# Optimization experiments

Measured on AMD Instinct MI355X. Metric: run time of the kernel, lower is better.

Reference implementation:

```python
import jax, jax.numpy as jnp
import numpy as np

S, M, E, K, C = 4096, 512, 16, 2, 128
H1, H2, H3 = 500, 500, 2000
SAMPLE = int(np.percentile(np.arange(S), 90))  # = 3685, matches int(np.percentile(idx_set, 90))
KMUL, KNUM = 2.0, 5


def setup_inputs() -> dict:
    key = jax.random.key(0)
    ks = jax.random.split(key, 8)
    def init(k, shape, fan):
        return (jax.random.normal(k, shape, jnp.float32) / np.float32(np.sqrt(fan)))
    inp = {
        'x': jax.random.normal(ks[0], (S, M), jnp.float32),
        'noise': jax.random.uniform(ks[1], (S, E), jnp.float32),
        'Wr': jnp.zeros((E, M), jnp.float32),  # router weight is zeroed in reset_parameters
        'W1': init(ks[2], (E, H1, M), M), 'b1': jnp.zeros((E, H1), jnp.float32),
        'W2': init(ks[3], (E, H2, H1), H1), 'b2': jnp.zeros((E, H2), jnp.float32),
        'W3': init(ks[4], (E, H3, H2), H2), 'b3': jnp.zeros((E, H3), jnp.float32),
        'W4': init(ks[5], (E, C, H3), H3), 'b4': jnp.zeros((E, C), jnp.float32),
    }
    rng = np.random.RandomState(0)
    npairs = K * (K - 1) // 2
    inp['idx1'] = jnp.asarray(np.stack([rng.choice(S, SAMPLE, replace=False) for _ in range(npairs)]).astype(np.int32))
    inp['idx2'] = jnp.asarray(np.stack([rng.choice(S, SAMPLE, replace=False) for _ in range(npairs)]).astype(np.int32))
    return inp


def _mmd(source, target):
    # Gaussian-kernel MMD, same math as MMD_loss (fix_sigma=None path).
    ns = source.shape[0]
    n = ns + target.shape[0]
    total = jnp.concatenate([source, target], axis=0)            # [n, d]
    sq = jnp.sum(total * total, axis=-1)
    d2 = sq[:, None] + sq[None, :] - 2.0 * (total @ total.T)     # [n, n] squared L2
    bw = jax.lax.stop_gradient(d2).sum() / (n * n - n)           # .data in torch => stop_gradient
    bw = bw / (KMUL ** (KNUM // 2))
    kern = jnp.zeros_like(d2)
    for i in range(KNUM):
        kern = kern + jnp.exp(-d2 / (bw * (KMUL ** i)))
    xx = kern[:ns, :ns]
    yy = kern[ns:, ns:]
    xy = kern[:ns, ns:]
    yx = kern[ns:, :ns]
    return jnp.mean(xx + yy - xy - yx)


def _forward(x, noise, Wr, W1, b1, W2, b2, W3, b3, W4, b4, idx1, idx2):
    select = x @ Wr.T + noise                                    # [S, E]
    gate, index = jax.lax.top_k(select, K)                       # [S, K]
    mask = jax.nn.one_hot(index, E, dtype=select.dtype)          # [S, K, E]
    density = mask.mean(axis=-2)                                 # [S, E]
    density_proxy = select.mean(axis=-2)                         # [E]
    balance_loss = jnp.mean(density_proxy * density) * float(E ** 2)
    mask_flat = mask.sum(axis=-1)                                # [S, K] (all ones)
    combine = jnp.transpose(gate[..., None] * mask_flat[..., None] * mask, (0, 2, 1))  # [S, E, K]
    dispatch = (combine != 0).astype(combine.dtype)              # bool().to(dtype)
    select0 = dispatch
    expert_inputs = jnp.einsum('sm,sec->ecm', x, dispatch)       # [E, K, M]
    h = jax.nn.relu(jnp.einsum('ecm,ehm->ech', expert_inputs, W1) + b1[:, None, :])
    h = jax.nn.relu(jnp.einsum('ech,egh->ecg', h, W2) + b2[:, None, :])
    h = jax.nn.relu(jnp.einsum('ecg,efg->ecf', h, W3) + b3[:, None, :])
    eout = jnp.einsum('ecf,edf->ecd', h, W4) + b4[:, None, :]    # [E, K, C]
    middle = jnp.transpose(jnp.einsum('sec,ecm->scm', combine, eout), (1, 0, 2))  # [K, S, C]
    output = jnp.einsum('sec,ecm->sm', combine, eout)            # [S, C]
    dist_loss = jnp.float32(0.0)
    p = 0
    for i in range(K):
        for j in range(i + 1, K):
            dist_loss = dist_loss - _mmd(middle[i][idx1[p]], middle[j][idx2[p]])
            p += 1
    return output, select0, balance_loss, dist_loss


def reference(x, noise, Wr, W1, b1, W2, b2, W3, b3, W4, b4, idx1, idx2):
    return _forward(x, noise, Wr, W1, b1, W2, b2, W3, b3, W4, b4, idx1, idx2)
```

## Files before the change

### kernel.cpp

```cpp
#include <hip/hip_runtime.h>

constexpr int S = 4096, M = 512, E = 16, CC = 128;
constexpr int H1 = 500, H2 = 500, H3 = 2000;
constexpr int TB = 256;

__global__ void k_route(const float* __restrict__ x, const float* __restrict__ noise,
                        const float* __restrict__ Wr, int* __restrict__ i0, int* __restrict__ i1,
                        float* __restrict__ g0, float* __restrict__ g1,
                        float* __restrict__ sel0, float* __restrict__ selpart,
                        int* __restrict__ counters) {
  if (blockIdx.x == 0 && threadIdx.x == 0) { counters[0] = 0; }
  int wid = threadIdx.x >> 6, lane = threadIdx.x & 63;
  int s = blockIdx.x * 4 + wid;
  const float* xr = x + (size_t)s * M;
  float xv[8];
#pragma unroll
  for (int c = 0; c < 8; ++c) xv[c] = xr[lane + 64 * c];
  float v[E];
#pragma unroll
  for (int e = 0; e < E; ++e) {
    const float* wr = Wr + (size_t)e * M;
    float acc = 0.f;
#pragma unroll
    for (int c = 0; c < 8; ++c) acc = fmaf(xv[c], wr[lane + 64 * c], acc);
#pragma unroll
    for (int off = 32; off; off >>= 1) acc += __shfl_xor(acc, off);
    v[e] = acc + noise[s * E + e];
  }
  int a0 = 0; float m0 = v[0];
#pragma unroll
  for (int e = 1; e < E; ++e) if (v[e] > m0) { m0 = v[e]; a0 = e; }
  int a1 = -1; float m1 = -3.4e38f;
#pragma unroll
  for (int e = 0; e < E; ++e) if (e != a0 && v[e] > m1) { m1 = v[e]; a1 = e; }
  __shared__ float vsh[4][16];
  if (lane < 16) vsh[wid][lane] = v[lane];
  if (lane == 0) { i0[s] = a0; i1[s] = a1; g0[s] = m0; g1[s] = m1; }
  if (lane < 16) {
    int e = lane;
    sel0[(size_t)s * 32 + e * 2 + 0] = (e == a0 && m0 != 0.f) ? 1.f : 0.f;
    sel0[(size_t)s * 32 + e * 2 + 1] = (e == a1 && m1 != 0.f) ? 1.f : 0.f;
  }
  __syncthreads();
  if (threadIdx.x < 16) {
    int e = threadIdx.x;
    selpart[blockIdx.x * 16 + e] = vsh[0][e] + vsh[1][e] + vsh[2][e] + vsh[3][e];
  }
}

__global__ void k_balance(const float* __restrict__ selpart, const int* __restrict__ i0,
                          const int* __restrict__ i1, float* __restrict__ outb) {
  __shared__ double part[512];
  __shared__ float dpl[E];
  int t = threadIdx.x;
  int e = t & 15, r0 = t >> 4;
  double acc = 0.0;
  for (int b = r0; b < 1024; b += 32) acc += (double)selpart[b * 16 + e];
  part[t] = acc;
  __syncthreads();
  for (int off = 256; off >= 16; off >>= 1) {
    if (t < off) part[t] += part[t + off];
    __syncthreads();
  }
  if (t < E) dpl[t] = (float)(part[t] / (double)S);
  __syncthreads();
  double acc2 = 0.0;
  for (int s = t; s < S; s += 512) acc2 += 0.5 * ((double)dpl[i0[s]] + (double)dpl[i1[s]]);
  part[t] = acc2;
  __syncthreads();
  for (int off = 256; off; off >>= 1) {
    if (t < off) part[t] += part[t + off];
    __syncthreads();
  }
  if (t == 0) outb[0] = (float)(part[0] / 256.0);
}

__global__ void k_lists(const int* __restrict__ i0, const int* __restrict__ i1,
                        const float* __restrict__ g0, const float* __restrict__ g1,
                        int* __restrict__ list, int* __restrict__ cnt) {
  int ek = blockIdx.x;
  int k = ek & 1, e = ek >> 1;
  const int* route = k ? i1 : i0;
  const float* gg = k ? g1 : g0;
  __shared__ int base_s;
  __shared__ int wsum[4];
  int t = threadIdx.x;
  int lane = t & 63, w = t >> 6;
  if (t == 0) base_s = 0;
  __syncthreads();
  for (int s0 = 0; s0 < S; s0 += 256) {
    int s = s0 + t;
    bool flag = (route[s] == e) && (gg[s] != 0.f);
    unsigned long long m = __ballot(flag);
    int within = __popcll(m & ((1ull << lane) - 1ull));
    if (lane == 0) wsum[w] = __popcll(m);
    __syncthreads();
    int wbase = base_s;
    for (int i = 0; i < w; ++i) wbase += wsum[i];
    if (flag) list[ek * S + wbase + within] = s;
    __syncthreads();
    if (t == 0) base_s += wsum[0] + wsum[1] + wsum[2] + wsum[3];
    __syncthreads();
  }
  if (t == 0) cnt[ek] = base_s;
}

__global__ void k_gather(const float* __restrict__ x, const int* __restrict__ list,
                         const int* __restrict__ cnt, float* __restrict__ gpart) {
  int b = blockIdx.x;
  int seg = b & 7, chunk = (b >> 3) & 3, ek = b >> 5;
  int t = threadIdx.x;
  int d = chunk * 128 + t;
  int nl = cnt[ek];
  const int* lp = list + ek * S;
  float acc = 0.f;
  int q = seg;
  for (; q + 24 < nl; q += 32) {
    int s0 = lp[q], s1 = lp[q + 8], s2 = lp[q + 16], s3 = lp[q + 24];
    acc += x[(size_t)s0 * M + d];
    acc += x[(size_t)s1 * M + d];
    acc += x[(size_t)s2 * M + d];
    acc += x[(size_t)s3 * M + d];
  }
  for (; q < nl; q += 8) acc += x[(size_t)lp[q] * M + d];
  gpart[(size_t)seg * (32 * M) + ek * M + d] = acc;
}

__global__ void k_gather_red(const float* __restrict__ gpart, float* __restrict__ ei) {
  int idx = blockIdx.x * blockDim.x + threadIdx.x;
  float acc = 0.f;
#pragma unroll
  for (int sg = 0; sg < 8; ++sg) acc += gpart[(size_t)sg * (32 * M) + idx];
  ei[idx] = acc;
}

template <int DIN, int HOUT, bool RELU>
__global__ void k_layer(const float* __restrict__ in, const float* __restrict__ W,
                        const float* __restrict__ bias, float* __restrict__ out) {
  int w = (blockIdx.x * blockDim.x + threadIdx.x) >> 6;
  int lane = threadIdx.x & 63;
  if (w >= E * HOUT) return;
  int e = w / HOUT, h = w - e * HOUT;
  const float* wr = W + ((size_t)e * HOUT + h) * DIN;
  const float* in0 = in + (size_t)(e * 2 + 0) * DIN;
  const float* in1 = in + (size_t)(e * 2 + 1) * DIN;
  float a0 = 0.f, a1 = 0.f;
  for (int m = lane; m < DIN; m += 64) {
    float wv = wr[m];
    a0 += wv * in0[m];
    a1 += wv * in1[m];
  }
#pragma unroll
  for (int off = 32; off; off >>= 1) {
    a0 += __shfl_xor(a0, off);
    a1 += __shfl_xor(a1, off);
  }
  if (lane == 0) {
    float bb = bias[e * HOUT + h];
    float o0 = a0 + bb, o1 = a1 + bb;
    if (RELU) { o0 = fmaxf(o0, 0.f); o1 = fmaxf(o1, 0.f); }
    out[(size_t)(e * 2 + 0) * HOUT + h] = o0;
    out[(size_t)(e * 2 + 1) * HOUT + h] = o1;
  }
}

__global__ void k_G(const float* __restrict__ eo, float* __restrict__ G32) {
  __shared__ float Es[32][129];
  int t = threadIdx.x;
  for (int i = t; i < 32 * 128; i += 256) Es[i >> 7][i & 127] = eo[i];
  __syncthreads();
  for (int p = t; p < 1024; p += 256) {
    int u = p >> 5, v = p & 31;
    float s = 0.f;
#pragma unroll 8
    for (int d = 0; d < 128; ++d) s = fmaf(Es[u][d], Es[v][d], s);
    G32[p] = s;
  }
}

__global__ void k_rows(const int* __restrict__ idx1, const int* __restrict__ idx2,
                       const int* __restrict__ i0, const int* __restrict__ i1,
                       const float* __restrict__ g0, const float* __restrict__ g1,
                       const float* __restrict__ G32, float* __restrict__ rowg,
                       float* __restrict__ rowa, int* __restrict__ rowe,
                       int ns, int ncnt, int npad) {
  int r = blockIdx.x * 256 + threadIdx.x;
  if (r >= npad) return;
  float g = 0.f; int ek = 0;
  if (r < ns)        { int t = idx1[r];      ek = i0[t] * 2 + 0; g = g0[t]; }
  else if (r < ncnt) { int t = idx2[r - ns]; ek = i1[t] * 2 + 1; g = g1[t]; }
  rowg[r] = g;
  rowe[r] = ek;
  rowa[r] = g * g * G32[ek * 32 + ek];
}

__global__ void k_prep(const float* __restrict__ rowg, const float* __restrict__ rowa,
                       const int* __restrict__ rowe, const float* __restrict__ G32,
                       float* __restrict__ cl, int ncnt) {
  __shared__ float ws[256 * 33];
  __shared__ double red[256];
  __shared__ float wfin[32];
  int t = threadIdx.x;
#pragma unroll
  for (int e = 0; e < 32; ++e) ws[t * 33 + e] = 0.f;
  double asum = 0.0;
  for (int r = t; r < ncnt; r += 256) {
    asum += (double)rowa[r];
    ws[t * 33 + rowe[r]] += rowg[r];
  }
  red[t] = asum;
  __syncthreads();
  if (t < 32) {
    float sw = 0.f;
    for (int q = 0; q < 256; ++q) sw += ws[q * 33 + t];
    wfin[t] = sw;
  }
  for (int off = 128; off; off >>= 1) { if (t < off) red[t] += red[t + off]; __syncthreads(); }
  double asum_tot = red[0];
  __syncthreads();
  double part = 0.0;
  for (int i = t; i < 1024; i += 256)
    part += (double)wfin[i >> 5] * (double)wfin[i & 31] * (double)G32[i];
  red[t] = part;
  __syncthreads();
  for (int off = 128; off; off >>= 1) { if (t < off) red[t] += red[t + off]; __syncthreads(); }
  if (t == 0) {
    double nn = (double)ncnt;
    double sumd2 = 2.0 * nn * asum_tot - 2.0 * red[0];
    double bw = sumd2 / (nn * nn - nn) / 4.0;
#pragma unroll
    for (int l = 0; l < 5; ++l) cl[l] = (float)(1.0 / (bw * (double)(1 << l)));
  }
}

__global__ __launch_bounds__(512) void k_mmd2(const float* __restrict__ rowg,
                      const float* __restrict__ rowa, const int* __restrict__ rowe,
                      const float* __restrict__ G32, const float* __restrict__ cl,
                      const float* __restrict__ eo,
                      const int* __restrict__ i0, const int* __restrict__ i1,
                      const float* __restrict__ g0, const float* __restrict__ g1,
                      float* __restrict__ out, double* __restrict__ bsum,
                      float* __restrict__ out_dist,
                      int ns, int ncnt, int nt, int ntri, int* __restrict__ counters) {
  int b = blockIdx.x, tid = threadIdx.x;
  if (b >= ntri) {
    int idx = (b - ntri) * 512 + tid;
    int s = idx >> 7, d = idx & (CC - 1);
    out[idx] = g0[s] * eo[(i0[s] * 2 + 0) * CC + d] + g1[s] * eo[(i1[s] * 2 + 1) * CC + d];
    return;
  }
  __shared__ float K2[1056];
  __shared__ float gA[264], aA[264], sA[264];
  __shared__ int   eA[264];
  __shared__ float gB[264], aB[264], sB[264];
  __shared__ int   eB[264];
  __shared__ float wred[8];
  __shared__ double redd[512];
  __shared__ int lastflag;

  int bi = 0, rem = b;
  while (rem >= nt - bi) { rem -= nt - bi; ++bi; }
  int bj = bi + rem;
  const int ib = bi * TB, jb = bj * TB;

  float c = cl[4];
  for (int i = tid; i < 1024; i += 512) K2[(i >> 5) * 33 + (i & 31)] = 2.f * c * G32[i];
  if (tid < TB) {
    int r = tid, p = (r & 7) * 33 + (r >> 3);
    int m = ib + r;
    gA[p] = rowg[m]; aA[p] = c * rowa[m]; eA[p] = rowe[m] * 33;
    sA[p] = (m < ns) ? 1.f : (m < ncnt ? -1.f : 0.f);
  } else {
    int r = tid - TB, p = (r & 7) * 33 + (r >> 3);
    int m = jb + r;
    gB[p] = rowg[m]; aB[p] = c * rowa[m]; eB[p] = rowe[m];
    sB[p] = (m < ns) ? 1.f : (m < ncnt ? -1.f : 0.f);
  }
  __syncthreads();

  int ti = tid & 15, tj = tid >> 4;
  float gj[8], Aj[8], sgj[8]; int exj[8];
#pragma unroll
  for (int q = 0; q < 8; ++q) {
    int p = q * 33 + tj;
    gj[q] = gB[p]; Aj[q] = aB[p]; exj[q] = eB[p]; sgj[q] = sB[p];
  }
  float gi[16], Ai[16], sgi[16]; int exi[16];
#pragma unroll
  for (int r = 0; r < 16; ++r) {
    int p = (r & 7) * 33 + ti * 2 + (r >> 3);
    gi[r] = gA[p]; Ai[r] = aA[p]; exi[r] = eA[p]; sgi[r] = sA[p];
  }

  float tsum = 0.f;
#pragma unroll
  for (int r = 0; r < 16; ++r) {
#pragma unroll
    for (int q = 0; q < 8; ++q) {
      float gg = gi[r] * gj[q];
      float arg = fmaf(K2[exi[r] + exj[q]], gg, -(Ai[r] + Aj[q]));
      float tv = __expf(arg);
      float t2 = tv * tv;   float s5 = tv + t2;
      float t4 = t2 * t2;   s5 += t4;
      float t8 = t4 * t4;   s5 += t8;
      float t16 = t8 * t8;  s5 += t16;
      tsum = fmaf(sgi[r] * sgj[q], s5, tsum);
    }
  }
#pragma unroll
  for (int off = 32; off; off >>= 1) tsum += __shfl_xor(tsum, off);
  if ((tid & 63) == 0) wred[tid >> 6] = tsum;
  __syncthreads();
  if (tid == 0) {
    float sblk = 0.f;
#pragma unroll
    for (int w = 0; w < 8; ++w) sblk += wred[w];
    bsum[b] = (double)sblk * ((bi == bj) ? 1.0 : 2.0);
  }

  if (tid == 0) {
    __threadfence();
    int old = atomicAdd(&counters[0], 1);
    lastflag = (old == ntri - 1) ? 1 : 0;
  }
  __syncthreads();
  if (!lastflag) return;
  __threadfence();
  double acc = 0.0;
  for (int i = tid; i < ntri; i += 512) acc += bsum[i];
  redd[tid] = acc;
  __syncthreads();
  for (int off = 256; off; off >>= 1) { if (tid < off) redd[tid] += redd[tid + off]; __syncthreads(); }
  if (tid == 0) out_dist[0] = (float)(-redd[0] / ((double)ns * (double)ns));
}

extern "C" void kernel_launch(void* const* d_in, const int* in_sizes, int n_in,
                              void* d_out, int out_size, void* d_ws, size_t ws_size,
                              hipStream_t stream) {
  const float* x  = (const float*)d_in[0];
  const float* noise = (const float*)d_in[1];
  const float* Wr = (const float*)d_in[2];
  const float* W1 = (const float*)d_in[3];
  const float* b1 = (const float*)d_in[4];
  const float* W2 = (const float*)d_in[5];
  const float* b2 = (const float*)d_in[6];
  const float* W3 = (const float*)d_in[7];
  const float* b3 = (const float*)d_in[8];
  const float* W4 = (const float*)d_in[9];
  const float* b4 = (const float*)d_in[10];
  const int* idx1 = (const int*)d_in[11];
  const int* idx2 = (const int*)d_in[12];
  int ns = in_sizes[11];
  int n = 2 * ns;
  int npad = (n + 255) & ~255;
  int nt = npad / TB;
  int ntri = nt * (nt + 1) / 2;

  char* wp = (char*)d_ws;
  size_t off = 0;
  auto alloc = [&](size_t bytes) -> void* {
    void* p = wp + off;
    off += (bytes + 255) & ~(size_t)255;
    return p;
  };
  int*   i0  = (int*)alloc((size_t)S * 4);
  int*   i1  = (int*)alloc((size_t)S * 4);
  float* g0  = (float*)alloc((size_t)S * 4);
  float* g1  = (float*)alloc((size_t)S * 4);
  float* selpart = (float*)alloc((size_t)1024 * 16 * 4);
  int*   list = (int*)alloc((size_t)32 * S * 4);
  int*   cnt  = (int*)alloc(32 * 4);
  float* gpart = (float*)alloc((size_t)8 * 32 * M * 4);
  float* ei  = (float*)alloc((size_t)E * 2 * M * 4);
  float* h1  = (float*)alloc((size_t)E * 2 * H1 * 4);
  float* h2  = (float*)alloc((size_t)E * 2 * H2 * 4);
  float* h3  = (float*)alloc((size_t)E * 2 * H3 * 4);
  float* eo  = (float*)alloc((size_t)E * 2 * CC * 4);
  float* G32 = (float*)alloc((size_t)1024 * 4);
  float* rowg = (float*)alloc((size_t)npad * 4);
  float* rowa = (float*)alloc((size_t)npad * 4);
  int*   rowe = (int*)alloc((size_t)npad * 4);
  float* cl  = (float*)alloc(8 * 4);
  double* bsum = (double*)alloc((size_t)ntri * 8);
  int* counters = (int*)alloc(256);
  (void)ws_size; (void)n_in; (void)out_size;

  float* out      = (float*)d_out;
  float* out_sel0 = out + (size_t)S * CC;
  float* out_bal  = out + (size_t)S * CC + (size_t)S * E * 2;
  float* out_dist = out_bal + 1;

  k_route<<<S / 4, 256, 0, stream>>>(x, noise, Wr, i0, i1, g0, g1, out_sel0, selpart, counters);
  k_balance<<<1, 512, 0, stream>>>(selpart, i0, i1, out_bal);
  k_lists<<<32, 256, 0, stream>>>(i0, i1, g0, g1, list, cnt);
  k_gather<<<1024, 128, 0, stream>>>(x, list, cnt, gpart);
  k_gather_red<<<64, 256, 0, stream>>>(gpart, ei);
  k_layer<M, H1, true><<<(E * H1 + 3) / 4, 256, 0, stream>>>(ei, W1, b1, h1);
  k_layer<H1, H2, true><<<(E * H2 + 3) / 4, 256, 0, stream>>>(h1, W2, b2, h2);
  k_layer<H2, H3, true><<<(E * H3 + 3) / 4, 256, 0, stream>>>(h2, W3, b3, h3);
  k_layer<H3, CC, false><<<(E * CC + 3) / 4, 256, 0, stream>>>(h3, W4, b4, eo);
  k_G<<<1, 256, 0, stream>>>(eo, G32);
  k_rows<<<(npad + 255) / 256, 256, 0, stream>>>(idx1, idx2, i0, i1, g0, g1, G32,
                                                 rowg, rowa, rowe, ns, n, npad);
  k_prep<<<1, 256, 0, stream>>>(rowg, rowa, rowe, G32, cl, n);
  k_mmd2<<<ntri + (S * CC) / 512, 512, 0, stream>>>(rowg, rowa, rowe, G32, cl, eo,
                                                    i0, i1, g0, g1, out, bsum, out_dist,
                                                    ns, n, nt, ntri, counters);
}
```

Measured before the change: 135.4 us.

## Fuse small reduction kernels using last-block atomic counters to cut launches

New measurement: 162.2 us. +19.7%, slower.

```diff
diff --git a/kernel.cpp b/kernel.cpp
--- a/kernel.cpp
+++ b/kernel.cpp
@@ -9,7 +9,7 @@
                         float* __restrict__ g0, float* __restrict__ g1,
                         float* __restrict__ sel0, float* __restrict__ selpart,
                         int* __restrict__ counters) {
-  if (blockIdx.x == 0 && threadIdx.x == 0) { counters[0] = 0; }
+  if (blockIdx.x == 0 && threadIdx.x < 4) counters[threadIdx.x] = 0;
   int wid = threadIdx.x >> 6, lane = threadIdx.x & 63;
   int s = blockIdx.x * 4 + wid;
   const float* xr = x + (size_t)s * M;
@@ -46,33 +46,6 @@
     int e = threadIdx.x;
     selpart[blockIdx.x * 16 + e] = vsh[0][e] + vsh[1][e] + vsh[2][e] + vsh[3][e];
   }
-}
-
-__global__ void k_balance(const float* __restrict__ selpart, const int* __restrict__ i0,
-                          const int* __restrict__ i1, float* __restrict__ outb) {
-  __shared__ double part[512];
-  __shared__ float dpl[E];
-  int t = threadIdx.x;
-  int e = t & 15, r0 = t >> 4;
-  double acc = 0.0;
-  for (int b = r0; b < 1024; b += 32) acc += (double)selpart[b * 16 + e];
-  part[t] = acc;
-  __syncthreads();
-  for (int off = 256; off >= 16; off >>= 1) {
-    if (t < off) part[t] += part[t + off];
-    __syncthreads();
-  }
-  if (t < E) dpl[t] = (float)(part[t] / (double)S);
-  __syncthreads();
-  double acc2 = 0.0;
-  for (int s = t; s < S; s += 512) acc2 += 0.5 * ((double)dpl[i0[s]] + (double)dpl[i1[s]]);
-  part[t] = acc2;
-  __syncthreads();
-  for (int off = 256; off; off >>= 1) {
-    if (t < off) part[t] += part[t + off];
-    __syncthreads();
-  }
-  if (t == 0) outb[0] = (float)(part[0] / 256.0);
 }
 
 __global__ void k_lists(const int* __restrict__ i0, const int* __restrict__ i1,
@@ -106,7 +79,8 @@
 }
 
 __global__ void k_gather(const float* __restrict__ x, const int* __restrict__ list,
-                         const int* __restrict__ cnt, float* __restrict__ gpart) {
+                         const int* __restrict__ cnt, float* __restrict__ gpart,
+                         float* __restrict__ ei, int* __restrict__ counters) {
   int b = blockIdx.x;
   int seg = b & 7, chunk = (b >> 3) & 3, ek = b >> 5;
   int t = threadIdx.x;
@@ -124,14 +98,28 @@
   }
   for (; q < nl; q += 8) acc += x[(size_t)lp[q] * M + d];
   gpart[(size_t)seg * (32 * M) + ek * M + d] = acc;
-}
-
-__global__ void k_gather_red(const float* __restrict__ gpart, float* __restrict__ ei) {
-  int idx = blockIdx.x * blockDim.x + threadIdx.x;
-  float acc = 0.f;
-#pragma unroll
-  for (int sg = 0; sg < 8; ++sg) acc += gpart[(size_t)sg * (32 * M) + idx];
-  ei[idx] = acc;
+
+  __shared__ int lastflag;
+  __syncthreads();
+  if (t == 0) {
+    __threadfence();
+    int old = atomicAdd(&counters[2], 1);
+    lastflag = (old == (int)gridDim.x - 1) ? 1 : 0;
+  }
+  __syncthreads();
+  if (!lastflag) return;
+  __threadfence();
+  const float4* gp4 = (const float4*)gpart;
+  float4* ei4 = (float4*)ei;
+  for (int i4 = t; i4 < (E * 2 * M) / 4; i4 += 128) {
+    float4 a = gp4[i4];
+#pragma unroll
+    for (int sg = 1; sg < 8; ++sg) {
+      float4 bb = gp4[(size_t)sg * ((32 * M) / 4) + i4];
+      a.x += bb.x; a.y += bb.y; a.z += bb.z; a.w += bb.w;
+    }
+    ei4[i4] = a;
+  }
 }
 
 template <int DIN, int HOUT, bool RELU>
@@ -164,69 +152,108 @@
   }
 }
 
-__global__ void k_G(const float* __restrict__ eo, float* __restrict__ G32) {
-  __shared__ float Es[32][129];
-  int t = threadIdx.x;
-  for (int i = t; i < 32 * 128; i += 256) Es[i >> 7][i & 127] = eo[i];
-  __syncthreads();
-  for (int p = t; p < 1024; p += 256) {
-    int u = p >> 5, v = p & 31;
-    float s = 0.f;
+__global__ __launch_bounds__(256) void k_mid2(const float* __restrict__ eo,
+                        const float* __restrict__ selpart,
+                        const int* __restrict__ idx1, const int* __restrict__ idx2,
+                        const int* __restrict__ i0, const int* __restrict__ i1,
+                        const float* __restrict__ g0, const float* __restrict__ g1,
+                        float* __restrict__ G32, float* __restrict__ rowg,
+                        float* __restrict__ rowa, int* __restrict__ rowe,
+                        float* __restrict__ wpart, float* __restrict__ cl,
+                        float* __restrict__ outb,
+                        int ns, int ncnt, int npad, int nrowblk, int* __restrict__ counters) {
+  __shared__ double redd[256];
+  __shared__ int lastflag;
+  int t = threadIdx.x, blk = blockIdx.x;
+  int lane = t & 63, w = t >> 6;
+
+  if (blk < nrowblk) {
+    __shared__ float diag[32];
+    __shared__ float sw[4][32], sw2[4][32];
+    if (t < 32) {
+      const float* er = eo + t * CC;
+      float s = 0.f;
+      for (int d = 0; d < CC; ++d) s = fmaf(er[d], er[d], s);
+      diag[t] = s;
+    }
+    __syncthreads();
+    int r = blk * 256 + t;
+    float g = 0.f; int ek = 0;
+    if (r < ns)        { int tk = idx1[r];      ek = i0[tk] * 2 + 0; g = g0[tk]; }
+    else if (r < ncnt) { int tk = idx2[r - ns]; ek = i1[tk] * 2 + 1; g = g1[tk]; }
+    if (r < npad) { rowg[r] = g; rowe[r] = ek; rowa[r] = g * g * diag[ek]; }
+    float g2 = g * g;
+    for (int e = 0; e < 32; ++e) {
+      float vw = (ek == e && r < npad) ? g : 0.f;
+      float vw2 = (ek == e && r < npad) ? g2 : 0.f;
+#pragma unroll
+      for (int off = 32; off; off >>= 1) { vw += __shfl_xor(vw, off); vw2 += __shfl_xor(vw2, off); }
+      if (lane == 0) { sw[w][e] = vw; sw2[w][e] = vw2; }
+    }
+    __syncthreads();
+    if (t < 32) {
+      wpart[blk * 64 + t]      = sw[0][t] + sw[1][t] + sw[2][t] + sw[3][t];
+      wpart[blk * 64 + 32 + t] = sw2[0][t] + sw2[1][t] + sw2[2][t] + sw2[3][t];
+    }
+  } else if (blk == nrowblk) {
+    __shared__ float Es[32 * 132];
+    for (int i = t; i < 32 * CC; i += 256) Es[(i >> 7) * 132 + (i & 127)] = eo[i];
+    __syncthreads();
+    for (int p = t; p < 1024; p += 256) {
+      int u = p >> 5, v = p & 31;
+      float s = 0.f;
 #pragma unroll 8
-    for (int d = 0; d < 128; ++d) s = fmaf(Es[u][d], Es[v][d], s);
-    G32[p] = s;
-  }
-}
-
-__global__ void k_rows(const int* __restrict__ idx1, const int* __restrict__ idx2,
-                       const int* __restrict__ i0, const int* __restrict__ i1,
-                       const float* __restrict__ g0, const float* __restrict__ g1,
-                       const float* __restrict__ G32, float* __restrict__ rowg,
-                       float* __restrict__ rowa, int* __restrict__ rowe,
-                       int ns, int ncnt, int npad) {
-  int r = blockIdx.x * 256 + threadIdx.x;
-  if (r >= npad) return;
-  float g = 0.f; int ek = 0;
-  if (r < ns)        { int t = idx1[r];      ek = i0[t] * 2 + 0; g = g0[t]; }
-  else if (r < ncnt) { int t = idx2[r - ns]; ek = i1[t] * 2 + 1; g = g1[t]; }
-  rowg[r] = g;
-  rowe[r] = ek;
-  rowa[r] = g * g * G32[ek * 32 + ek];
-}
-
-__global__ void k_prep(const float* __restrict__ rowg, const float* __restrict__ rowa,
-                       const int* __restrict__ rowe, const float* __restrict__ G32,
-                       float* __restrict__ cl, int ncnt) {
-  __shared__ float ws[256 * 33];
-  __shared__ double red[256];
-  __shared__ float wfin[32];
-  int t = threadIdx.x;
-#pragma unroll
-  for (int e = 0; e < 32; ++e) ws[t * 33 + e] = 0.f;
-  double asum = 0.0;
-  for (int r = t; r < ncnt; r += 256) {
-    asum += (double)rowa[r];
-    ws[t * 33 + rowe[r]] += rowg[r];
-  }
-  red[t] = asum;
-  __syncthreads();
+      for (int d = 0; d < CC; ++d) s = fmaf(Es[u * 132 + d], Es[v * 132 + d], s);
+      G32[p] = s;
+    }
+  } else {
+    __shared__ float dpl[16];
+    int e2 = t & 15, r0 = t >> 4;
+    double acc = 0.0;
+    for (int b2 = r0; b2 < 1024; b2 += 16) acc += (double)selpart[b2 * 16 + e2];
+    redd[t] = acc;
+    __syncthreads();
+    for (int off = 128; off >= 16; off >>= 1) { if (t < off) redd[t] += redd[t + off]; __syncthreads(); }
+    if (t < 16) dpl[t] = (float)(redd[t] / (double)S);
+    __syncthreads();
+    double acc2 = 0.0;
+    for (int s2 = t; s2 < S; s2 += 256) acc2 += 0.5 * ((double)dpl[i0[s2]] + (double)dpl[i1[s2]]);
+    redd[t] = acc2;
+    __syncthreads();
+    for (int off = 128; off; off >>= 1) { if (t < off) redd[t] += redd[t + off]; __syncthreads(); }
+    if (t == 0) outb[0] = (float)(redd[0] / 256.0);
+  }
+
+  __syncthreads();
+  if (t == 0) {
+    __threadfence();
+    int old = atomicAdd(&counters[1], 1);
+    lastflag = (old == nrowblk + 2 - 1) ? 1 : 0;
+  }
+  __syncthreads();
+  if (!lastflag) return;
+  __threadfence();
+  __shared__ float wf[32], w2f[32];
   if (t < 32) {
-    float sw = 0.f;
-    for (int q = 0; q < 256; ++q) sw += ws[q * 33 + t];
-    wfin[t] = sw;
-  }
-  for (int off = 128; off; off >>= 1) { if (t < off) red[t] += red[t + off]; __syncthreads(); }
-  double asum_tot = red[0];
+    float sw = 0.f, sw2 = 0.f;
+    for (int b = 0; b < nrowblk; ++b) { sw += wpart[b * 64 + t]; sw2 += wpart[b * 64 + 32 + t]; }
+    wf[t] = sw; w2f[t] = sw2;
+  }
   __syncthreads();
   double part = 0.0;
   for (int i = t; i < 1024; i += 256)
-    part += (double)wfin[i >> 5] * (double)wfin[i & 31] * (double)G32[i];
-  red[t] = part;
-  __syncthreads();
-  for (int off = 128; off; off >>= 1) { if (t < off) red[t] += red[t + off]; __syncthreads(); }
+    part += (double)wf[i >> 5] * (double)wf[i & 31] * (double)G32[i];
+  redd[t] = part;
+  __syncthreads();
+  for (int off = 128; off; off >>= 1) { if (t < off) redd[t] += redd[t + off]; __syncthreads(); }
+  double wGw = redd[0];
+  __syncthreads();
+  redd[t] = (t < 32) ? (double)w2f[t] * (double)G32[t * 33] : 0.0;
+  __syncthreads();
+  for (int off = 128; off; off >>= 1) { if (t < off) redd[t] += redd[t + off]; __syncthreads(); }
   if (t == 0) {
     double nn = (double)ncnt;
-    double sumd2 = 2.0 * nn * asum_tot - 2.0 * red[0];
+    double sumd2 = 2.0 * nn * redd[0] - 2.0 * wGw;
     double bw = sumd2 / (nn * nn - nn) / 4.0;
 #pragma unroll
     for (int l = 0; l < 5; ++l) cl[l] = (float)(1.0 / (bw * (double)(1 << l)));
@@ -355,6 +382,7 @@
   int npad = (n + 255) & ~255;
   int nt = npad / TB;
   int ntri = nt * (nt + 1) / 2;
+  int nrowblk = npad / 256;
 
   char* wp = (char*)d_ws;
   size_t off = 0;
@@ -380,6 +408,7 @@
   float* rowg = (float*)alloc((size_t)npad * 4);
   float* rowa = (float*)alloc((size_t)npad * 4);
   int*   rowe = (int*)alloc((size_t)npad * 4);
+  float* wpart = (float*)alloc((size_t)nrowblk * 64 * 4);
   float* cl  = (float*)alloc(8 * 4);
   double* bsum = (double*)alloc((size_t)ntri * 8);
   int* counters = (int*)alloc(256);
@@ -391,18 +420,15 @@
   float* out_dist = out_bal + 1;
 
   k_route<<<S / 4, 256, 0, stream>>>(x, noise, Wr, i0, i1, g0, g1, out_sel0, selpart, counters);
-  k_balance<<<1, 512, 0, stream>>>(selpart, i0, i1, out_bal);
   k_lists<<<32, 256, 0, stream>>>(i0, i1, g0, g1, list, cnt);
-  k_gather<<<1024, 128, 0, stream>>>(x, list, cnt, gpart);
-  k_gather_red<<<64, 256, 0, stream>>>(gpart, ei);
+  k_gather<<<1024, 128, 0, stream>>>(x, list, cnt, gpart, ei, counters);
   k_layer<M, H1, true><<<(E * H1 + 3) / 4, 256, 0, stream>>>(ei, W1, b1, h1);
   k_layer<H1, H2, true><<<(E * H2 + 3) / 4, 256, 0, stream>>>(h1, W2, b2, h2);
   k_layer<H2, H3, true><<<(E * H3 + 3) / 4, 256, 0, stream>>>(h2, W3, b3, h3);
   k_layer<H3, CC, false><<<(E * CC + 3) / 4, 256, 0, stream>>>(h3, W4, b4, eo);
-  k_G<<<1, 256, 0, stream>>>(eo, G32);
-  k_rows<<<(npad + 255) / 256, 256, 0, stream>>>(idx1, idx2, i0, i1, g0, g1, G32,
-                                                 rowg, rowa, rowe, ns, n, npad);
-  k_prep<<<1, 256, 0, stream>>>(rowg, rowa, rowe, G32, cl, n);
+  k_mid2<<<nrowblk + 2, 256, 0, stream>>>(eo, selpart, idx1, idx2, i0, i1, g0, g1,
+                                          G32, rowg, rowa, rowe, wpart, cl, out_bal,
+                                          ns, n, npad, nrowblk, counters);
   k_mmd2<<<ntri + (S * CC) / 512, 512, 0, stream>>>(rowg, rowa, rowe, G32, cl, eo,
                                                     i0, i1, g0, g1, out, bsum, out_dist,
                                                     ns, n, nt, ntri, counters);
```
